# Kernel optimization log

Measured on AMD Instinct MI355X. Metric: run time of the kernel, lower is better.

Reference implementation:

```python
import jax, jax.numpy as jnp
import numpy as np

B, T, D, H = 4, 2048, 1024, 16
Dh = D // H

def setup_inputs() -> dict:
    key = jax.random.key(0)
    ks = jax.random.split(key, 6)
    scale = 1.0 / np.sqrt(D)
    return {
        "x": jax.random.normal(ks[0], (B, T, D), dtype=jnp.float32),
        "W_q": jax.random.normal(ks[1], (D, D), dtype=jnp.float32) * scale,
        "W_k": jax.random.normal(ks[2], (D, D), dtype=jnp.float32) * scale,
        "W_v": jax.random.normal(ks[3], (D, D), dtype=jnp.float32) * scale,
        "W_o": jax.random.normal(ks[4], (D, D), dtype=jnp.float32) * scale,
        "b_o": jax.random.normal(ks[5], (D,), dtype=jnp.float32) * 0.02,
    }

def reference(x, W_q, W_k, W_v, W_o, b_o):
    # Linear weights stored torch-style (out, in): y = x @ W.T
    def split_heads(z):
        return z.reshape(B, T, H, Dh).transpose(0, 2, 1, 3)  # [B,H,T,Dh]
    q = split_heads(x @ W_q.T)
    k = split_heads(x @ W_k.T)
    v = split_heads(x @ W_v.T)
    scale = Dh ** -0.5
    attn = jnp.einsum('bhqd,bhkd->bhqk', q, k) * scale  # [B,H,T,T]
    causal = jnp.tril(jnp.ones((T, T), dtype=bool))
    attn = jnp.where(causal[None, None], attn, -jnp.inf)
    attn = jax.nn.softmax(attn, axis=-1)
    y = jnp.einsum('bhqk,bhkd->bhqd', attn, v)  # [B,H,T,Dh]
    y = y.transpose(0, 2, 1, 3).reshape(B, T, D)
    return y @ W_o.T + b_o
```

## Files before the change

### kernel.cpp

```cpp
#include <hip/hip_runtime.h>
#include <hip/hip_bf16.h>
#include <stdint.h>

#define B_   4
#define T_   2048
#define H_   16
#define MTOT (B_ * T_)
#define NQKV 3072
#define QSC  0.18033688f

typedef __attribute__((ext_vector_type(8))) __bf16 bf16x8;
typedef __attribute__((ext_vector_type(4))) float f32x4;
typedef __attribute__((ext_vector_type(16))) float f32x16;
typedef __attribute__((ext_vector_type(4))) float f4v;
typedef __attribute__((ext_vector_type(4))) unsigned short us4;
typedef __attribute__((ext_vector_type(8))) unsigned short us8;
typedef __attribute__((ext_vector_type(4))) unsigned int u32x4;

static __device__ __forceinline__ unsigned short f2bf(float f) {
  __hip_bfloat16 h = __float2bfloat16(f);
  return __builtin_bit_cast(unsigned short, h);
}

static __device__ __forceinline__ float fast_exp2(float x) {
#if __has_builtin(__builtin_amdgcn_exp2f)
  return __builtin_amdgcn_exp2f(x);
#else
  float r; asm("v_exp_f32 %0, %1" : "=v"(r) : "v"(x)); return r;
#endif
}

static __device__ __forceinline__ void async16(const void* g, void* l) {
  __builtin_amdgcn_global_load_lds(
      (const __attribute__((address_space(1))) void*)g,
      (__attribute__((address_space(3))) void*)l, 16, 0, 0);
}

#define XHALF(res, x, OP)                                  \
  {                                                        \
    float t1_ = (x), t2_ = (x);                            \
    asm("" : "+v"(t2_));                                   \
    asm("v_permlane32_swap_b32 %0, %1" : "+v"(t1_), "+v"(t2_)); \
    res = OP(t1_, t2_);                                    \
  }
static __device__ __forceinline__ float fadd_(float a, float b) { return a + b; }

__global__ __launch_bounds__(256) void cvt_all(
    const float* __restrict__ x, const float* __restrict__ Wq,
    const float* __restrict__ Wk, const float* __restrict__ Wv,
    const float* __restrict__ Wo, unsigned short* __restrict__ xb,
    unsigned short* __restrict__ wqkv, unsigned short* __restrict__ wo) {
  int i = blockIdx.x * blockDim.x + threadIdx.x;
  const float* s; unsigned short* d; int j;
  if (i < 2097152)      { s = x;  d = xb;             j = i; }
  else if (i < 2359296) { s = Wq; d = wqkv;           j = i - 2097152; }
  else if (i < 2621440) { s = Wk; d = wqkv + 1048576; j = i - 2359296; }
  else if (i < 2883584) { s = Wv; d = wqkv + 2097152; j = i - 2621440; }
  else                  { s = Wo; d = wo;             j = i - 2883584; }
  f4v v = reinterpret_cast<const f4v*>(s)[j];
  us4 o;
  o.x = f2bf(v.x); o.y = f2bf(v.y); o.z = f2bf(v.z); o.w = f2bf(v.w);
  reinterpret_cast<us4*>(d)[j] = o;
}

__global__ __launch_bounds__(512) void gemm_qkv(
    const unsigned short* __restrict__ A,
    const unsigned short* __restrict__ Bw,
    unsigned short* __restrict__ Cb) {
  const int K = 1024;
  __shared__ __align__(16) unsigned short As[128 * 64];
  __shared__ __align__(16) unsigned short Bs[256 * 64];

  const int bid = blockIdx.x;
  const int xcd = bid & 7;
  const int loc = bid >> 3;
  const int m0 = (xcd * 8 + loc / 12) * 128;
  const int n0 = (loc % 12) * 256;

  const int t = threadIdx.x;
  const int lane = t & 63;
  const int w = t >> 6;
  const int lr = lane & 15;
  const int lg = lane >> 4;
  const int wm = w >> 2;
  const int wn = w & 3;

  f32x4 acc[4][4];
#pragma unroll
  for (int i = 0; i < 4; ++i)
#pragma unroll
    for (int j = 0; j < 4; ++j) acc[i][j] = (f32x4){0.f, 0.f, 0.f, 0.f};

  const int srow = t >> 3;
  const int gs = (t & 7) ^ (srow & 7);
  const unsigned short* ga = A + (size_t)(m0 + srow) * K + gs * 8;
  const unsigned short* gb = Bw + (size_t)(n0 + srow) * K + gs * 8;
  const int rsw = lr & 7;

  for (int k0 = 0; k0 < K; k0 += 64) {
#pragma unroll
    for (int k = 0; k < 2; ++k)
      async16(ga + (size_t)(k * 64) * K + k0, &As[(k * 512 + t) * 8]);
#pragma unroll
    for (int k = 0; k < 4; ++k)
      async16(gb + (size_t)(k * 64) * K + k0, &Bs[(k * 512 + t) * 8]);
    __syncthreads();

#pragma unroll
    for (int kk = 0; kk < 2; ++kk) {
      const int slot = ((kk * 4 + lg) ^ rsw) * 8;
      bf16x8 af[4], bfr[4];
#pragma unroll
      for (int mi = 0; mi < 4; ++mi)
        af[mi] = *(const bf16x8*)&As[(wm * 64 + mi * 16 + lr) * 64 + slot];
#pragma unroll
      for (int ni = 0; ni < 4; ++ni)
        bfr[ni] = *(const bf16x8*)&Bs[(wn * 64 + ni * 16 + lr) * 64 + slot];
#pragma unroll
      for (int mi = 0; mi < 4; ++mi)
#pragma unroll
        for (int ni = 0; ni < 4; ++ni)
          acc[mi][ni] = __builtin_amdgcn_mfma_f32_16x16x32_bf16(
              af[mi], bfr[ni], acc[mi][ni], 0, 0, 0);
    }
    __syncthreads();
  }

#pragma unroll
  for (int mi = 0; mi < 4; ++mi) {
    const int row = m0 + wm * 64 + mi * 16 + lg * 4;
#pragma unroll
    for (int ni = 0; ni < 4; ++ni) {
      const int col = n0 + wn * 64 + ni * 16 + lr;
      const float sc = (col < 1024) ? QSC : 1.0f;
#pragma unroll
      for (int r = 0; r < 4; ++r)
        Cb[(size_t)(row + r) * NQKV + col] = f2bf(acc[mi][ni][r] * sc);
    }
  }
}

template <int NT>
__global__ __launch_bounds__(256) void gemm_bt(
    const unsigned short* __restrict__ A,
    const unsigned short* __restrict__ Bw,
    float* __restrict__ Cf,
    const float* __restrict__ bias,
    int K, int N) {
  __shared__ __align__(16) unsigned short As[128 * 64];
  __shared__ __align__(16) unsigned short Bs[128 * 64];

  const int bid = blockIdx.x;
  const int xcd = bid & 7;
  const int loc = bid >> 3;
  const int m0 = (xcd * 8 + loc / NT) * 128;
  const int n0 = (loc % NT) * 128;

  const int t = threadIdx.x;
  const int lane = t & 63;
  const int w = t >> 6;
  const int lr = lane & 15;
  const int lg = lane >> 4;
  const int wm = w >> 1;
  const int wn = w & 1;

  f32x4 acc[4][4];
#pragma unroll
  for (int i = 0; i < 4; ++i)
#pragma unroll
    for (int j = 0; j < 4; ++j) acc[i][j] = (f32x4){0.f, 0.f, 0.f, 0.f};

  const int srow = t >> 3;
  const int gs = (t & 7) ^ ((t >> 3) & 7);
  const unsigned short* ga = A + (size_t)(m0 + srow) * K + gs * 8;
  const unsigned short* gb = Bw + (size_t)(n0 + srow) * K + gs * 8;

  const int rsw = lr & 7;

  for (int k0 = 0; k0 < K; k0 += 64) {
#pragma unroll
    for (int k = 0; k < 4; ++k) {
      async16(ga + (size_t)(k * 32) * K + k0, &As[(k * 256 + t) * 8]);
      async16(gb + (size_t)(k * 32) * K + k0, &Bs[(k * 256 + t) * 8]);
    }
    __syncthreads();

#pragma unroll
    for (int kk = 0; kk < 2; ++kk) {
      const int slot = ((kk * 4 + lg) ^ rsw) * 8;
      bf16x8 af[4], bfr[4];
#pragma unroll
      for (int mi = 0; mi < 4; ++mi)
        af[mi] = *(const bf16x8*)&As[(wm * 64 + mi * 16 + lr) * 64 + slot];
#pragma unroll
      for (int ni = 0; ni < 4; ++ni)
        bfr[ni] = *(const bf16x8*)&Bs[(wn * 64 + ni * 16 + lr) * 64 + slot];
#pragma unroll
      for (int mi = 0; mi < 4; ++mi)
#pragma unroll
        for (int ni = 0; ni < 4; ++ni)
          acc[mi][ni] = __builtin_amdgcn_mfma_f32_16x16x32_bf16(
              af[mi], bfr[ni], acc[mi][ni], 0, 0, 0);
    }
    __syncthreads();
  }

#pragma unroll
  for (int mi = 0; mi < 4; ++mi) {
    const int row = m0 + wm * 64 + mi * 16 + lg * 4;
#pragma unroll
    for (int ni = 0; ni < 4; ++ni) {
      const int col = n0 + wn * 64 + ni * 16 + lr;
#pragma unroll
      for (int r = 0; r < 4; ++r)
        Cf[(size_t)(row + r) * N + col] = acc[mi][ni][r] + bias[col];
    }
  }
}

__global__ __launch_bounds__(256, 4) void attn_kernel(
    const unsigned short* __restrict__ qkv, unsigned short* __restrict__ ob) {
  const int bid = blockIdx.x;
  const int pair = bid & 63;
  const int g = bid >> 6;
  const int rnd = g >> 2, idx = g & 3;
  const int qg = (rnd == 0) ? (15 - idx)
               : (rnd == 1) ? (8 + idx)
               : (rnd == 2) ? (7 - idx) : idx;
  const int b = pair >> 4;
  const int h = pair & 15;
  const int t = threadIdx.x;
  const int w = t >> 6;
  const int lane = t & 63;
  const int l31 = lane & 31;
  const int hi = lane >> 5;

  const int q0w = qg * 128 + w * 32;
  const int myBound = 2 * qg + (w >> 1);
  const int NT = 2 * qg + 2;

  __shared__ __align__(16) unsigned short Ks[2][64 * 64];
  __shared__ __align__(16) unsigned short Vs[2][64 * 64];

  const size_t rowbase = (size_t)(b * T_) * NQKV;

  bf16x8 Qf[4];
  {
    const unsigned short* qp =
        qkv + rowbase + (size_t)(q0w + l31) * NQKV + h * 64 + hi * 8;
#pragma unroll
    for (int m = 0; m < 4; ++m) Qf[m] = *(const bf16x8*)(qp + m * 16);
  }

  const int kr = t >> 3;
  const int ks = t & 7;
  const unsigned short* kbase =
      qkv + rowbase + 1024 + h * 64 + (ks ^ (kr & 7)) * 8 + (size_t)kr * NQKV;
  const int kvr = t >> 2;
  const int dc2 = (t & 3) * 2;
  const unsigned short* vbase =
      qkv + rowbase + 2048 + h * 64 + dc2 * 8 + (size_t)kvr * NQKV;

  float m_i = -INFINITY, l_i = 0.f;
  f32x16 o[2];
#pragma unroll
  for (int r = 0; r < 16; ++r) { o[0][r] = 0.f; o[1][r] = 0.f; }

#define VSCATTER(Vb, v0, v1)                                       \
  {                                                                \
    _Pragma("unroll") for (int i = 0; i < 8; ++i) {                \
      const int s0 = ((kvr >> 3) ^ dc2 ^ i) & 7;                   \
      const int s1 = ((kvr >> 3) ^ (dc2 + 1) ^ i) & 7;             \
      (Vb)[(dc2 * 8 + i) * 64 + s0 * 8 + (kvr & 7)] = (v0)[i];     \
      (Vb)[((dc2 + 1) * 8 + i) * 64 + s1 * 8 + (kvr & 7)] = (v1)[i]; \
    }                                                              \
  }

  {
    async16(kbase, &Ks[0][t * 8]);
    async16(kbase + (size_t)32 * NQKV, &Ks[0][2048 + t * 8]);
    us8 v0 = *(const us8*)vbase;
    us8 v1 = *(const us8*)(vbase + 8);
    VSCATTER(&Vs[0][0], v0, v1);
  }

  int cur = 0;
  for (int kt = 0; kt < NT; ++kt) {
    __syncthreads();

    const bool pf = (kt + 1 < NT);
    us8 v0, v1;
    if (pf) {
      const size_t off = (size_t)(kt + 1) * 64 * NQKV;
      async16(kbase + off, &Ks[cur ^ 1][t * 8]);
      async16(kbase + off + (size_t)32 * NQKV, &Ks[cur ^ 1][2048 + t * 8]);
      v0 = *(const us8*)(vbase + off);
      v1 = *(const us8*)(vbase + off + 8);
    }

    if (kt <= myBound) {
      const unsigned short* Kb = Ks[cur];
      const unsigned short* Vb = Vs[cur];

      f32x16 a0, a1;
#pragma unroll
      for (int r = 0; r < 16; ++r) { a0[r] = 0.f; a1[r] = 0.f; }
      {
        const int rb0 = l31 * 64;
        const int rb1 = (32 + l31) * 64;
        const int r7 = l31 & 7;
        __builtin_amdgcn_s_setprio(1);
#pragma unroll
        for (int m = 0; m < 4; ++m) {
          const int c = (((m << 1) | hi) ^ r7) * 8;
          bf16x8 kf0 = *(const bf16x8*)&Kb[rb0 + c];
          bf16x8 kf1 = *(const bf16x8*)&Kb[rb1 + c];
          a0 = __builtin_amdgcn_mfma_f32_32x32x16_bf16(kf0, Qf[m], a0, 0, 0, 0);
          a1 = __builtin_amdgcn_mfma_f32_32x32x16_bf16(kf1, Qf[m], a1, 0, 0, 0);
        }
        __builtin_amdgcn_s_setprio(0);
      }

      if (kt == myBound) {
        const int qglob = q0w + l31;
#pragma unroll
        for (int r = 0; r < 16; ++r) {
          const int kvb = kt * 64 + (r & 3) + ((r >> 2) << 3) + (hi << 2);
          if (kvb > qglob) a0[r] = -INFINITY;
          if (kvb + 32 > qglob) a1[r] = -INFINITY;
        }
      }

      float m8[8];
#pragma unroll
      for (int j2 = 0; j2 < 8; ++j2)
        m8[j2] = fmaxf(fmaxf(a0[j2], a0[j2 + 8]), fmaxf(a1[j2], a1[j2 + 8]));
      float pp = fmaxf(fmaxf(fmaxf(m8[0], m8[4]), fmaxf(m8[1], m8[5])),
                       fmaxf(fmaxf(m8[2], m8[6]), fmaxf(m8[3], m8[7])));
      float pmax;
      XHALF(pmax, pp, fmaxf);
      if (__any(pmax > m_i + 8.f)) {
        const float mnew = fmaxf(m_i, pmax);
        const float al = fast_exp2(m_i - mnew);
        m_i = mnew;
        l_i *= al;
#pragma unroll
        for (int r = 0; r < 16; ++r) { o[0][r] *= al; o[1][r] *= al; }
      }

#pragma unroll
      for (int r = 0; r < 16; ++r) {
        a0[r] = fast_exp2(a0[r] - m_i);
        a1[r] = fast_exp2(a1[r] - m_i);
      }
      float s8[8];
#pragma unroll
      for (int j2 = 0; j2 < 8; ++j2)
        s8[j2] = (a0[j2] + a0[j2 + 8]) + (a1[j2] + a1[j2 + 8]);
      float rp = ((s8[0] + s8[1]) + (s8[2] + s8[3])) +
                 ((s8[4] + s8[5]) + (s8[6] + s8[7]));
      float rs;
      XHALF(rs, rp, fadd_);
      l_i += rs;

      bf16x8 Pf[4];
#pragma unroll
      for (int m = 0; m < 4; ++m) {
        const int rb2 = (m & 1) * 8;
        uint32_t u0, u1, u2, u3;
        const f32x16& s = (m >> 1) ? a1 : a0;
        asm("v_cvt_pk_bf16_f32 %0, %1, %2" : "=v"(u0) : "v"(s[rb2 + 0]), "v"(s[rb2 + 1]));
        asm("v_cvt_pk_bf16_f32 %0, %1, %2" : "=v"(u1) : "v"(s[rb2 + 2]), "v"(s[rb2 + 3]));
        asm("v_cvt_pk_bf16_f32 %0, %1, %2" : "=v"(u2) : "v"(s[rb2 + 4]), "v"(s[rb2 + 5]));
        asm("v_cvt_pk_bf16_f32 %0, %1, %2" : "=v"(u3) : "v"(s[rb2 + 6]), "v"(s[rb2 + 7]));
        asm("v_permlane32_swap_b32 %0, %1" : "+v"(u0), "+v"(u2));
        asm("v_permlane32_swap_b32 %0, %1" : "+v"(u1), "+v"(u3));
        u32x4 pw = {u0, u1, u2, u3};
        Pf[m] = __builtin_bit_cast(bf16x8, pw);
      }

      __builtin_amdgcn_s_setprio(1);
#pragma unroll
      for (int dt = 0; dt < 2; ++dt) {
        const int d = dt * 32 + l31;
        const int base = d * 64;
        const int dsw = ((d >> 3) ^ d) & 7;
#pragma unroll
        for (int m = 0; m < 4; ++m) {
          bf16x8 vf = *(const bf16x8*)&Vb[base + ((((m << 1) | hi) ^ dsw) & 7) * 8];
          o[dt] = __builtin_amdgcn_mfma_f32_32x32x16_bf16(vf, Pf[m], o[dt], 0, 0, 0);
        }
      }
      __builtin_amdgcn_s_setprio(0);
    }

    if (pf) VSCATTER(&Vs[cur ^ 1][0], v0, v1);
    cur ^= 1;
  }

  const float rl = 1.0f / l_i;
#pragma unroll
  for (int dt = 0; dt < 2; ++dt) {
    float s[16];
#pragma unroll
    for (int r = 0; r < 16; ++r) s[r] = o[dt][r] * rl;
    uint32_t u[8];
#pragma unroll
    for (int p = 0; p < 8; ++p)
      asm("v_cvt_pk_bf16_f32 %0, %1, %2" : "=v"(u[p]) : "v"(s[2 * p]), "v"(s[2 * p + 1]));
    asm("v_permlane32_swap_b32 %0, %1" : "+v"(u[0]), "+v"(u[2]));
    asm("v_permlane32_swap_b32 %0, %1" : "+v"(u[1]), "+v"(u[3]));
    asm("v_permlane32_swap_b32 %0, %1" : "+v"(u[4]), "+v"(u[6]));
    asm("v_permlane32_swap_b32 %0, %1" : "+v"(u[5]), "+v"(u[7]));
    unsigned short* op =
        ob + (size_t)(b * T_ + q0w + l31) * 1024 + h * 64 + dt * 32 + hi * 8;
    u32x4 c0 = {u[0], u[1], u[2], u[3]};
    u32x4 c1 = {u[4], u[5], u[6], u[7]};
    *(u32x4*)op = c0;
    *(u32x4*)(op + 16) = c1;
  }
}

extern "C" void kernel_launch(void* const* d_in, const int* in_sizes, int n_in,
                              void* d_out, int out_size, void* d_ws,
                              size_t ws_size, hipStream_t stream) {
  const float* x = (const float*)d_in[0];
  const float* Wq = (const float*)d_in[1];
  const float* Wk = (const float*)d_in[2];
  const float* Wv = (const float*)d_in[3];
  const float* Wo = (const float*)d_in[4];
  const float* bo = (const float*)d_in[5];
  float* out = (float*)d_out;

  char* ws = (char*)d_ws;
  unsigned short* xb   = (unsigned short*)(ws + 0);
  unsigned short* wqkv = (unsigned short*)(ws + 16777216);
  unsigned short* wo   = (unsigned short*)(ws + 23068672);
  unsigned short* qkv  = (unsigned short*)(ws + 25165824);
  unsigned short* ob   = (unsigned short*)(ws + 75497472);
  if (ws_size < 92274688u) return;

  cvt_all<<<12288, 256, 0, stream>>>(x, Wq, Wk, Wv, Wo, xb, wqkv, wo);

  gemm_qkv<<<768, 512, 0, stream>>>(xb, wqkv, qkv);

  attn_kernel<<<dim3(1024), 256, 0, stream>>>(qkv, ob);

  gemm_bt<8><<<512, 256, 0, stream>>>(ob, wo, out, bo, 1024, 1024);
}
```

Baseline: 158.0 us.

## Write V transposed from QKV GEMM so attention loads V tiles asynchronously

The QKV projection epilogue now writes V in a transposed [H*Dh, B*T] layout while Q and K go to a separate 2048-wide buffer. The attention kernel can then fetch V tiles with the same async 16-byte global-to-LDS copies used for K, with an XOR swizzle. This replaces the per-element register scatter into shared memory. The cost is strided transposed 8-byte stores in the GEMM epilogue for the V columns.

After: 154.2 us. -2.4%, faster.

```diff
diff --git a/kernel.cpp b/kernel.cpp
--- a/kernel.cpp
+++ b/kernel.cpp
@@ -6,7 +6,7 @@
 #define T_   2048
 #define H_   16
 #define MTOT (B_ * T_)
-#define NQKV 3072
+#define NQK  2048
 #define QSC  0.18033688f
 
 typedef __attribute__((ext_vector_type(8))) __bf16 bf16x8;
@@ -66,7 +66,8 @@
 __global__ __launch_bounds__(512) void gemm_qkv(
     const unsigned short* __restrict__ A,
     const unsigned short* __restrict__ Bw,
-    unsigned short* __restrict__ Cb) {
+    unsigned short* __restrict__ Cqk,
+    unsigned short* __restrict__ vT) {
   const int K = 1024;
   __shared__ __align__(16) unsigned short As[128 * 64];
   __shared__ __align__(16) unsigned short Bs[256 * 64];
@@ -126,16 +127,31 @@
     __syncthreads();
   }
 
-#pragma unroll
-  for (int mi = 0; mi < 4; ++mi) {
-    const int row = m0 + wm * 64 + mi * 16 + lg * 4;
-#pragma unroll
-    for (int ni = 0; ni < 4; ++ni) {
-      const int col = n0 + wn * 64 + ni * 16 + lr;
-      const float sc = (col < 1024) ? QSC : 1.0f;
-#pragma unroll
-      for (int r = 0; r < 4; ++r)
-        Cb[(size_t)(row + r) * NQKV + col] = f2bf(acc[mi][ni][r] * sc);
+  if (n0 < 2048) {
+#pragma unroll
+    for (int mi = 0; mi < 4; ++mi) {
+      const int row = m0 + wm * 64 + mi * 16 + lg * 4;
+#pragma unroll
+      for (int ni = 0; ni < 4; ++ni) {
+        const int col = n0 + wn * 64 + ni * 16 + lr;
+        const float sc = (col < 1024) ? QSC : 1.0f;
+#pragma unroll
+        for (int r = 0; r < 4; ++r)
+          Cqk[(size_t)(row + r) * NQK + col] = f2bf(acc[mi][ni][r] * sc);
+      }
+    }
+  } else {
+#pragma unroll
+    for (int mi = 0; mi < 4; ++mi) {
+      const int row = m0 + wm * 64 + mi * 16 + lg * 4;
+#pragma unroll
+      for (int ni = 0; ni < 4; ++ni) {
+        const int col2 = (n0 - 2048) + wn * 64 + ni * 16 + lr;
+        us4 pk;
+#pragma unroll
+        for (int r = 0; r < 4; ++r) pk[r] = f2bf(acc[mi][ni][r]);
+        *(us4*)&vT[(size_t)col2 * 8192 + row] = pk;
+      }
     }
   }
 }
@@ -219,7 +235,8 @@
 }
 
 __global__ __launch_bounds__(256, 4) void attn_kernel(
-    const unsigned short* __restrict__ qkv, unsigned short* __restrict__ ob) {
+    const unsigned short* __restrict__ qk, const unsigned short* __restrict__ vT,
+    unsigned short* __restrict__ ob) {
   const int bid = blockIdx.x;
   const int pair = bid & 63;
   const int g = bid >> 6;
@@ -242,65 +259,52 @@
   __shared__ __align__(16) unsigned short Ks[2][64 * 64];
   __shared__ __align__(16) unsigned short Vs[2][64 * 64];
 
-  const size_t rowbase = (size_t)(b * T_) * NQKV;
+  const size_t rowbase = (size_t)(b * T_) * NQK;
 
   bf16x8 Qf[4];
   {
     const unsigned short* qp =
-        qkv + rowbase + (size_t)(q0w + l31) * NQKV + h * 64 + hi * 8;
+        qk + rowbase + (size_t)(q0w + l31) * NQK + h * 64 + hi * 8;
 #pragma unroll
     for (int m = 0; m < 4; ++m) Qf[m] = *(const bf16x8*)(qp + m * 16);
   }
 
   const int kr = t >> 3;
-  const int ks = t & 7;
+  const int gsw = ((t & 7) ^ (kr & 7)) * 8;
   const unsigned short* kbase =
-      qkv + rowbase + 1024 + h * 64 + (ks ^ (kr & 7)) * 8 + (size_t)kr * NQKV;
-  const int kvr = t >> 2;
-  const int dc2 = (t & 3) * 2;
+      qk + rowbase + 1024 + h * 64 + gsw + (size_t)kr * NQK;
   const unsigned short* vbase =
-      qkv + rowbase + 2048 + h * 64 + dc2 * 8 + (size_t)kvr * NQKV;
+      vT + (size_t)(h * 64 + kr) * 8192 + (size_t)(b * T_) + gsw;
 
   float m_i = -INFINITY, l_i = 0.f;
   f32x16 o[2];
 #pragma unroll
   for (int r = 0; r < 16; ++r) { o[0][r] = 0.f; o[1][r] = 0.f; }
 
-#define VSCATTER(Vb, v0, v1)                                       \
-  {                                                                \
-    _Pragma("unroll") for (int i = 0; i < 8; ++i) {                \
-      const int s0 = ((kvr >> 3) ^ dc2 ^ i) & 7;                   \
-      const int s1 = ((kvr >> 3) ^ (dc2 + 1) ^ i) & 7;             \
-      (Vb)[(dc2 * 8 + i) * 64 + s0 * 8 + (kvr & 7)] = (v0)[i];     \
-      (Vb)[((dc2 + 1) * 8 + i) * 64 + s1 * 8 + (kvr & 7)] = (v1)[i]; \
-    }                                                              \
-  }
-
   {
     async16(kbase, &Ks[0][t * 8]);
-    async16(kbase + (size_t)32 * NQKV, &Ks[0][2048 + t * 8]);
-    us8 v0 = *(const us8*)vbase;
-    us8 v1 = *(const us8*)(vbase + 8);
-    VSCATTER(&Vs[0][0], v0, v1);
+    async16(kbase + (size_t)32 * NQK, &Ks[0][2048 + t * 8]);
+    async16(vbase, &Vs[0][t * 8]);
+    async16(vbase + (size_t)32 * 8192, &Vs[0][2048 + t * 8]);
   }
 
   int cur = 0;
   for (int kt = 0; kt < NT; ++kt) {
     __syncthreads();
 
-    const bool pf = (kt + 1 < NT);
-    us8 v0, v1;
-    if (pf) {
-      const size_t off = (size_t)(kt + 1) * 64 * NQKV;
-      async16(kbase + off, &Ks[cur ^ 1][t * 8]);
-      async16(kbase + off + (size_t)32 * NQKV, &Ks[cur ^ 1][2048 + t * 8]);
-      v0 = *(const us8*)(vbase + off);
-      v1 = *(const us8*)(vbase + off + 8);
+    if (kt + 1 < NT) {
+      const size_t ko = (size_t)(kt + 1) * 64 * NQK;
+      const size_t vo = (size_t)(kt + 1) * 64;
+      async16(kbase + ko, &Ks[cur ^ 1][t * 8]);
+      async16(kbase + ko + (size_t)32 * NQK, &Ks[cur ^ 1][2048 + t * 8]);
+      async16(vbase + vo, &Vs[cur ^ 1][t * 8]);
+      async16(vbase + vo + (size_t)32 * 8192, &Vs[cur ^ 1][2048 + t * 8]);
     }
 
     if (kt <= myBound) {
       const unsigned short* Kb = Ks[cur];
       const unsigned short* Vb = Vs[cur];
+      const int r7 = l31 & 7;
 
       f32x16 a0, a1;
 #pragma unroll
@@ -308,7 +312,6 @@
       {
         const int rb0 = l31 * 64;
         const int rb1 = (32 + l31) * 64;
-        const int r7 = l31 & 7;
         __builtin_amdgcn_s_setprio(1);
 #pragma unroll
         for (int m = 0; m < 4; ++m) {
@@ -382,19 +385,17 @@
       __builtin_amdgcn_s_setprio(1);
 #pragma unroll
       for (int dt = 0; dt < 2; ++dt) {
-        const int d = dt * 32 + l31;
-        const int base = d * 64;
-        const int dsw = ((d >> 3) ^ d) & 7;
+        const int base = (dt * 32 + l31) * 64;
 #pragma unroll
         for (int m = 0; m < 4; ++m) {
-          bf16x8 vf = *(const bf16x8*)&Vb[base + ((((m << 1) | hi) ^ dsw) & 7) * 8];
+          const int c = (((m << 1) | hi) ^ r7) * 8;
+          bf16x8 vf = *(const bf16x8*)&Vb[base + c];
           o[dt] = __builtin_amdgcn_mfma_f32_32x32x16_bf16(vf, Pf[m], o[dt], 0, 0, 0);
         }
       }
       __builtin_amdgcn_s_setprio(0);
     }
 
-    if (pf) VSCATTER(&Vs[cur ^ 1][0], v0, v1);
     cur ^= 1;
   }
 
@@ -436,15 +437,16 @@
   unsigned short* xb   = (unsigned short*)(ws + 0);
   unsigned short* wqkv = (unsigned short*)(ws + 16777216);
   unsigned short* wo   = (unsigned short*)(ws + 23068672);
-  unsigned short* qkv  = (unsigned short*)(ws + 25165824);
+  unsigned short* qk   = (unsigned short*)(ws + 25165824);
+  unsigned short* vT   = (unsigned short*)(ws + 58720256);
   unsigned short* ob   = (unsigned short*)(ws + 75497472);
   if (ws_size < 92274688u) return;
 
   cvt_all<<<12288, 256, 0, stream>>>(x, Wq, Wk, Wv, Wo, xb, wqkv, wo);
 
-  gemm_qkv<<<768, 512, 0, stream>>>(xb, wqkv, qkv);
-
-  attn_kernel<<<dim3(1024), 256, 0, stream>>>(qkv, ob);
+  gemm_qkv<<<768, 512, 0, stream>>>(xb, wqkv, qk, vT);
+
+  attn_kernel<<<dim3(1024), 256, 0, stream>>>(qk, vT, ob);
 
   gemm_bt<8><<<512, 256, 0, stream>>>(ob, wo, out, bo, 1024, 1024);
 }
```
